# Performance work log

Measured on AMD Instinct MI355X. Metric: run time of the kernel, lower is better.

The kernel has to match this reference:

```python
import jax, jax.numpy as jnp
import numpy as np

DIM = 1024

def setup_inputs() -> dict:
    key = jax.random.key(0)
    k1, k2, k3, k4 = jax.random.split(key, 4)
    B, L, D = 32, 2048, DIM
    x = jax.random.normal(k1, (B, D), dtype=jnp.float32)
    context = jax.random.normal(k2, (B, L, D), dtype=jnp.float32)
    # linear_concatWa: Linear(2*dim, dim, bias=False) -> weight [dim, 2*dim]
    Wa = jax.random.normal(k3, (D, 2 * D), dtype=jnp.float32) * (1.0 / np.sqrt(2 * D))
    # linear_concatVa: Linear(dim, 1, bias=False) -> weight [1, dim]
    Va = jax.random.normal(k4, (1, D), dtype=jnp.float32) * (1.0 / np.sqrt(D))
    return {"x": x, "context": context, "Wa": Wa, "Va": Va}


def reference(x, context, Wa, Va):
    # concat-mode additive (Bahdanau) attention.
    # Wa @ cat(ht, hs) == ht @ Wa[:, :D].T + hs @ Wa[:, D:].T  (avoids materializing concat)
    D = x.shape[-1]
    Wa_t, Wa_s = Wa[:, :D], Wa[:, D:]              # each [D, D]
    ht_proj = jnp.einsum('bd,kd->bk', x, Wa_t)     # [B, D]
    hs_proj = jnp.einsum('bld,kd->blk', context, Wa_s)  # [B, L, D]
    hidden = jnp.tanh(ht_proj[:, None, :] + hs_proj)    # [B, L, D]
    scores = jnp.einsum('blk,ok->bl', hidden, Va)       # [B, L]  (Va: [1, D])
    attn = jax.nn.softmax(scores, axis=-1)               # [B, L]
    weighted = jnp.einsum('bl,bld->bd', attn, context)   # [B, D]
    return weighted, attn
```

## Files before the change

### kernel.cpp

```cpp
#include <hip/hip_runtime.h>
#include <hip/hip_bf16.h>
#include <cstdint>
#include <cstddef>

#define DIM 1024
#define B_SZ 32
#define L_SZ 2048

#define BM 128
#define BN 128

#define CVT_BLOCKS 8192
#define HT_BLOCKS  512
#define WA_BLOCKS  512

typedef __attribute__((ext_vector_type(8))) short bf16x8;
typedef __attribute__((ext_vector_type(4))) float floatx4;

static __device__ __forceinline__ unsigned cvt2_bf16_rne(float a, float b) {
    unsigned ua = __builtin_bit_cast(unsigned, a);
    unsigned ub = __builtin_bit_cast(unsigned, b);
    ua = (ua + 0x7FFFu + ((ua >> 16) & 1u)) >> 16;
    ub = (ub + 0x7FFFu + ((ub >> 16) & 1u)) >> 16;
    return ua | (ub << 16);
}

static __device__ __forceinline__ float bf2f(unsigned u16) {
    return __builtin_bit_cast(float, u16 << 16);
}

static __device__ __forceinline__ float tanh_fast(float x) {
    float e = __expf(2.0f * x);
    return 1.0f - 2.0f * __builtin_amdgcn_rcpf(e + 1.0f);
}

static __device__ __forceinline__ void gld_lds16(const void* g, void* lds) {
    __builtin_amdgcn_global_load_lds(
        (const __attribute__((address_space(1))) unsigned int*)g,
        (__attribute__((address_space(3))) unsigned int*)lds,
        16, 0, 0);
}

__global__ __launch_bounds__(256) void pre_kernel(
    const float* __restrict__ x, const float* __restrict__ ctx,
    const float* __restrict__ Wa,
    unsigned short* __restrict__ ctxB, unsigned short* __restrict__ WaB,
    float* __restrict__ ht, float* __restrict__ scores,
    float* __restrict__ weighted)
{
    const int bid = blockIdx.x, t = threadIdx.x;

    if (bid < CVT_BLOCKS) {
        const float4* c4 = (const float4*)ctx;
        uint2* o2 = (uint2*)ctxB;
        #pragma unroll
        for (int it = 0; it < 4; ++it) {
            const long g = ((long)it * CVT_BLOCKS + bid) * 512;
            const float4 a = c4[g + t];
            const float4 b = c4[g + 256 + t];
            o2[g + t]       = make_uint2(cvt2_bf16_rne(a.x, a.y), cvt2_bf16_rne(a.z, a.w));
            o2[g + 256 + t] = make_uint2(cvt2_bf16_rne(b.x, b.y), cvt2_bf16_rne(b.z, b.w));
        }
    } else if (bid < CVT_BLOCKS + HT_BLOCKS) {
        const int lb = bid - CVT_BLOCKS;
        const int gi = lb * 256 + t;
        if (gi < B_SZ * L_SZ) scores[gi] = 0.f;
        const int b = lb >> 4, kb = lb & 15;
        __shared__ float xs[DIM];
        for (int i = t; i < DIM; i += 256) xs[i] = x[b * DIM + i];
        __syncthreads();
        const int wave = t >> 6, lane = t & 63;
        const float4* xs4 = (const float4*)xs;
        for (int kk = 0; kk < 16; ++kk) {
            const int k = kb * 64 + wave * 16 + kk;
            const float4* wr = (const float4*)(Wa + (size_t)k * (2 * DIM));
            float s = 0.f;
            #pragma unroll
            for (int d = 0; d < DIM / 4; d += 64) {
                const float4 w4 = wr[d + lane];
                const float4 x4 = xs4[d + lane];
                s += w4.x * x4.x + w4.y * x4.y + w4.z * x4.z + w4.w * x4.w;
            }
            #pragma unroll
            for (int off = 32; off > 0; off >>= 1) s += __shfl_xor(s, off);
            if (lane == 0) ht[b * DIM + k] = s;
        }
    } else {
        const int lb = bid - CVT_BLOCKS - HT_BLOCKS;
        const int i = lb * 256 + t;
        if (i < B_SZ * DIM) weighted[i] = 0.f;
        const int k = i >> 7, dc = i & 127;
        const float* s = Wa + (size_t)k * (2 * DIM) + DIM + dc * 8;
        const float4 a = ((const float4*)s)[0];
        const float4 b4 = ((const float4*)s)[1];
        uint4 o;
        o.x = cvt2_bf16_rne(a.x, a.y);
        o.y = cvt2_bf16_rne(a.z, a.w);
        o.z = cvt2_bf16_rne(b4.x, b4.y);
        o.w = cvt2_bf16_rne(b4.z, b4.w);
        ((uint4*)(WaB + (size_t)k * DIM + dc * 8))[0] = o;
    }
}

__global__ __launch_bounds__(256) void gemm_score_bf16(
    const unsigned short* __restrict__ A, const unsigned short* __restrict__ Bm,
    const float* __restrict__ Va, const float* __restrict__ ht,
    float* __restrict__ scores)
{
    __shared__ __align__(16) unsigned short As[BM * 64];
    __shared__ __align__(16) unsigned short Bs[BN * 64];
    const int t = threadIdx.x;

    const int bid = blockIdx.x;
    const int logical = (bid & 7) * 512 + (bid >> 3);
    const int n0 = (logical & 7) * BN;
    const int m0 = (logical >> 3) * BM;

    const int lane = t & 63, wave = t >> 6;
    const int l15 = lane & 15, quad = lane >> 4;
    const int wm = (wave >> 1) * 64, wn = (wave & 1) * 64;

    const int lr = lane >> 3;
    const int lc = (lane & 7) ^ lr;
    const size_t aRow = (size_t)(m0 + wave * 32 + lr);
    const size_t bRow = (size_t)(n0 + wave * 32 + lr);

    floatx4 acc[4][4];
    #pragma unroll
    for (int i = 0; i < 4; ++i)
        #pragma unroll
        for (int j = 0; j < 4; ++j) acc[i][j] = (floatx4)0.f;

    for (int k0 = 0; k0 < DIM; k0 += 64) {
        #pragma unroll
        for (int q = 0; q < 4; ++q) {
            gld_lds16(A + (aRow + q * 8) * DIM + k0 + lc * 8,
                      &As[(wave * 32 + q * 8) * 64]);
            gld_lds16(Bm + (bRow + q * 8) * DIM + k0 + lc * 8,
                      &Bs[(wave * 32 + q * 8) * 64]);
        }
        __syncthreads();

        bf16x8 af[2][4], bv[2][4];
        #pragma unroll
        for (int kb = 0; kb < 2; ++kb) {
            #pragma unroll
            for (int i = 0; i < 4; ++i) {
                const int r = wm + i * 16 + l15;
                const int c = (kb * 4 + quad) ^ (r & 7);
                af[kb][i] = *(const bf16x8*)&As[r * 64 + c * 8];
            }
            #pragma unroll
            for (int j = 0; j < 4; ++j) {
                const int r = wn + j * 16 + l15;
                const int c = (kb * 4 + quad) ^ (r & 7);
                bv[kb][j] = *(const bf16x8*)&Bs[r * 64 + c * 8];
            }
        }
        #pragma unroll
        for (int kb = 0; kb < 2; ++kb)
            #pragma unroll
            for (int i = 0; i < 4; ++i)
                #pragma unroll
                for (int j = 0; j < 4; ++j)
                    acc[i][j] = __builtin_amdgcn_mfma_f32_16x16x32_bf16(
                        af[kb][i], bv[kb][j], acc[i][j], 0, 0, 0);
        __syncthreads();
    }

    const int bb = m0 >> 11;
    float htv[4], vav[4];
    #pragma unroll
    for (int j = 0; j < 4; ++j) {
        const int ng = n0 + wn + j * 16 + l15;
        htv[j] = ht[bb * DIM + ng];
        vav[j] = Va[ng];
    }
    #pragma unroll
    for (int i = 0; i < 4; ++i) {
        #pragma unroll
        for (int r = 0; r < 4; ++r) {
            float s = 0.f;
            #pragma unroll
            for (int j = 0; j < 4; ++j)
                s += tanh_fast(acc[i][j][r] + htv[j]) * vav[j];
            s += __shfl_xor(s, 8);
            s += __shfl_xor(s, 4);
            s += __shfl_xor(s, 2);
            s += __shfl_xor(s, 1);
            if (l15 == 0)
                atomicAdd(&scores[m0 + wm + i * 16 + quad * 4 + r], s);
        }
    }
}

__global__ __launch_bounds__(256) void stats_kernel(
    const float* __restrict__ scores, float* __restrict__ attn)
{
    const int b = blockIdx.x, t = threadIdx.x;
    const float* sc = scores + b * L_SZ;
    __shared__ float red[256];

    float m = -1e30f;
    for (int l = t; l < L_SZ; l += 256) m = fmaxf(m, sc[l]);
    red[t] = m; __syncthreads();
    for (int s = 128; s > 0; s >>= 1) { if (t < s) red[t] = fmaxf(red[t], red[t + s]); __syncthreads(); }
    m = red[0]; __syncthreads();
    float sum = 0.f;
    for (int l = t; l < L_SZ; l += 256) sum += __expf(sc[l] - m);
    red[t] = sum; __syncthreads();
    for (int s = 128; s > 0; s >>= 1) { if (t < s) red[t] += red[t + s]; __syncthreads(); }
    const float inv = 1.0f / red[0];

    for (int l = t; l < L_SZ; l += 256)
        attn[b * L_SZ + l] = __expf(sc[l] - m) * inv;
}

__global__ __launch_bounds__(256) void post_kernel(
    const float* __restrict__ attn, const unsigned short* __restrict__ ctxB,
    float* __restrict__ weighted)
{
    const int b = blockIdx.x, slice = blockIdx.y, t = threadIdx.x;
    __shared__ float att[128];
    const int l0 = slice * 128;
    if (t < 128) att[t] = attn[b * L_SZ + l0 + t];
    __syncthreads();

    const unsigned short* cb = ctxB + ((size_t)b * L_SZ + l0) * DIM + t * 4;
    float a0 = 0.f, a1 = 0.f, a2 = 0.f, a3 = 0.f;
    #pragma unroll 4
    for (int l = 0; l < 128; ++l) {
        const float a = att[l];
        const uint2 v = *(const uint2*)(cb + (size_t)l * DIM);
        a0 += a * bf2f(v.x & 0xFFFFu);
        a1 += a * bf2f(v.x >> 16);
        a2 += a * bf2f(v.y & 0xFFFFu);
        a3 += a * bf2f(v.y >> 16);
    }
    float* o = weighted + b * DIM + t * 4;
    atomicAdd(o + 0, a0);
    atomicAdd(o + 1, a1);
    atomicAdd(o + 2, a2);
    atomicAdd(o + 3, a3);
}

#define LDS_STRIDE 40
__global__ __launch_bounds__(256) void ht_kernel_fb(const float* __restrict__ x,
                                                    const float* __restrict__ Wa,
                                                    float* __restrict__ ht,
                                                    float* __restrict__ scores,
                                                    float* __restrict__ weighted) {
    const int b = blockIdx.x, kb = blockIdx.y, t = threadIdx.x;
    const int gidx = (b * 16 + kb) * 256 + t;
    if (gidx < B_SZ * L_SZ) scores[gidx] = 0.f;
    if (gidx < B_SZ * DIM) weighted[gidx] = 0.f;
    __shared__ float xs[DIM];
    for (int i = t; i < DIM; i += 256) xs[i] = x[b * DIM + i];
    __syncthreads();
    const int wave = t >> 6, lane = t & 63;
    for (int kk = 0; kk < 16; ++kk) {
        const int k = kb * 64 + wave * 16 + kk;
        const float* wr = Wa + (size_t)k * (2 * DIM);
        float s = 0.f;
        #pragma unroll
        for (int d = 0; d < DIM; d += 64) s += xs[d + lane] * wr[d + lane];
        #pragma unroll
        for (int off = 32; off > 0; off >>= 1) s += __shfl_xor(s, off);
        if (lane == 0) ht[b * DIM + k] = s;
    }
}

__global__ __launch_bounds__(256, 2) void gemm_score_kernel(
    const float* __restrict__ ctx, const float* __restrict__ Wa,
    const float* __restrict__ Va, const float* __restrict__ ht,
    float* __restrict__ scores)
{
    __shared__ unsigned short As[BM * LDS_STRIDE];
    __shared__ unsigned short Bs[BN * LDS_STRIDE];
    const int t = threadIdx.x;
    const int n0 = blockIdx.x * BN;
    const int m0 = blockIdx.y * BM;
    const int lane = t & 63, wave = t >> 6;
    const int l15 = lane & 15, quad = lane >> 4;
    const int wm = (wave >> 1) * 64, wn = (wave & 1) * 64;
    const int srow = t >> 3;
    const int scol = (t & 7) * 4;
    const float* aBase = ctx + (size_t)(m0 + srow) * DIM + scol;
    const float* bBase = Wa + (size_t)(n0 + srow) * (2 * DIM) + DIM + scol;

    floatx4 acc[4][4];
    #pragma unroll
    for (int i = 0; i < 4; ++i)
        #pragma unroll
        for (int j = 0; j < 4; ++j) acc[i][j] = (floatx4)0.f;

    for (int k0 = 0; k0 < DIM; k0 += 32) {
        __syncthreads();
        #pragma unroll
        for (int r = 0; r < 4; ++r) {
            const float4 va = *(const float4*)(aBase + (size_t)(r * 32) * DIM + k0);
            const float4 vb = *(const float4*)(bBase + (size_t)(r * 32) * (2 * DIM) + k0);
            *(uint2*)&As[(srow + r * 32) * LDS_STRIDE + scol] =
                make_uint2(cvt2_bf16_rne(va.x, va.y), cvt2_bf16_rne(va.z, va.w));
            *(uint2*)&Bs[(srow + r * 32) * LDS_STRIDE + scol] =
                make_uint2(cvt2_bf16_rne(vb.x, vb.y), cvt2_bf16_rne(vb.z, vb.w));
        }
        __syncthreads();
        bf16x8 af[4], bfr[4];
        #pragma unroll
        for (int i = 0; i < 4; ++i)
            af[i] = *(const bf16x8*)&As[(wm + i * 16 + l15) * LDS_STRIDE + quad * 8];
        #pragma unroll
        for (int j = 0; j < 4; ++j)
            bfr[j] = *(const bf16x8*)&Bs[(wn + j * 16 + l15) * LDS_STRIDE + quad * 8];
        #pragma unroll
        for (int i = 0; i < 4; ++i)
            #pragma unroll
            for (int j = 0; j < 4; ++j)
                acc[i][j] = __builtin_amdgcn_mfma_f32_16x16x32_bf16(af[i], bfr[j], acc[i][j], 0, 0, 0);
    }
    const int bb = m0 >> 11;
    float htv[4], vav[4];
    #pragma unroll
    for (int j = 0; j < 4; ++j) {
        const int ng = n0 + wn + j * 16 + l15;
        htv[j] = ht[bb * DIM + ng];
        vav[j] = Va[ng];
    }
    #pragma unroll
    for (int i = 0; i < 4; ++i) {
        #pragma unroll
        for (int r = 0; r < 4; ++r) {
            float s = 0.f;
            #pragma unroll
            for (int j = 0; j < 4; ++j)
                s += tanh_fast(acc[i][j][r] + htv[j]) * vav[j];
            s += __shfl_xor(s, 8);
            s += __shfl_xor(s, 4);
            s += __shfl_xor(s, 2);
            s += __shfl_xor(s, 1);
            if (l15 == 0)
                atomicAdd(&scores[m0 + wm + i * 16 + quad * 4 + r], s);
        }
    }
}

__global__ __launch_bounds__(256) void post_kernel_fb(
    const float* __restrict__ scores, const float* __restrict__ ctx,
    float* __restrict__ attn, float* __restrict__ weighted)
{
    const int b = blockIdx.x, slice = blockIdx.y, t = threadIdx.x;
    const float* sc = scores + b * L_SZ;
    __shared__ float red[256];
    __shared__ float att[128];
    float m = -1e30f;
    for (int l = t; l < L_SZ; l += 256) m = fmaxf(m, sc[l]);
    red[t] = m; __syncthreads();
    for (int s = 128; s > 0; s >>= 1) { if (t < s) red[t] = fmaxf(red[t], red[t + s]); __syncthreads(); }
    m = red[0]; __syncthreads();
    float sum = 0.f;
    for (int l = t; l < L_SZ; l += 256) sum += __expf(sc[l] - m);
    red[t] = sum; __syncthreads();
    for (int s = 128; s > 0; s >>= 1) { if (t < s) red[t] += red[t + s]; __syncthreads(); }
    const float inv = 1.0f / red[0];
    const int l0 = slice * 128;
    if (t < 128) {
        const float av = __expf(sc[l0 + t] - m) * inv;
        att[t] = av;
        attn[b * L_SZ + l0 + t] = av;
    }
    __syncthreads();
    const float* cb = ctx + ((size_t)b * L_SZ + l0) * DIM + t * 4;
    float4 w = make_float4(0.f, 0.f, 0.f, 0.f);
    for (int l = 0; l < 128; ++l) {
        const float a = att[l];
        const float4 c = *(const float4*)(cb + (size_t)l * DIM);
        w.x += a * c.x; w.y += a * c.y; w.z += a * c.z; w.w += a * c.w;
    }
    float* o = weighted + b * DIM + t * 4;
    atomicAdd(o + 0, w.x);
    atomicAdd(o + 1, w.y);
    atomicAdd(o + 2, w.z);
    atomicAdd(o + 3, w.w);
}

extern "C" void kernel_launch(void* const* d_in, const int* in_sizes, int n_in,
                              void* d_out, int out_size, void* d_ws, size_t ws_size,
                              hipStream_t stream) {
    const float* x   = (const float*)d_in[0];
    const float* ctx = (const float*)d_in[1];
    const float* Wa  = (const float*)d_in[2];
    const float* Va  = (const float*)d_in[3];

    float* out      = (float*)d_out;
    float* weighted = out;
    float* attn     = out + B_SZ * DIM;

    float* scores = (float*)d_ws;
    float* ht     = scores + B_SZ * L_SZ;

    const size_t base = (size_t)(B_SZ * L_SZ + B_SZ * DIM) * sizeof(float);
    const size_t need = base + (size_t)DIM * DIM * 2
                      + (size_t)B_SZ * L_SZ * DIM * 2;

    if (ws_size >= need) {
        unsigned short* WaB  = (unsigned short*)((char*)d_ws + base);
        unsigned short* ctxB = WaB + (size_t)DIM * DIM;
        pre_kernel<<<CVT_BLOCKS + HT_BLOCKS + WA_BLOCKS, 256, 0, stream>>>(
            x, ctx, Wa, ctxB, WaB, ht, scores, weighted);
        gemm_score_bf16<<<(DIM / BN) * ((B_SZ * L_SZ) / BM), 256, 0, stream>>>(
            ctxB, WaB, Va, ht, scores);
        stats_kernel<<<B_SZ, 256, 0, stream>>>(scores, attn);
        post_kernel<<<dim3(B_SZ, 16), 256, 0, stream>>>(attn, ctxB, weighted);
    } else {
        ht_kernel_fb<<<dim3(B_SZ, 16), 256, 0, stream>>>(x, Wa, ht, scores, weighted);
        gemm_score_kernel<<<dim3(DIM / BN, (B_SZ * L_SZ) / BM), 256, 0, stream>>>(
            ctx, Wa, Va, ht, scores);
        post_kernel_fb<<<dim3(B_SZ, 16), 256, 0, stream>>>(scores, ctx, attn, weighted);
    }
}
```

Baseline: 607.5 us.

## Double-buffer LDS tiles in bf16 score GEMM and drop block swizzle

Splits the GEMM's shared-memory tiles into two buffers, so global-to-LDS loads for the next K slice are issued before the MFMA work on the current slice. This hides load latency behind compute. It also removes the XCD-aware block index remapping and launches a plain 2D grid, which changes L2 locality across chiplets. The kernel now uses twice the LDS (64KB), which may lower occupancy.

```diff
diff --git a/kernel.cpp b/kernel.cpp
--- a/kernel.cpp
+++ b/kernel.cpp
@@ -102,20 +102,58 @@
     }
 }
 
+#define STAGE(AS, BS, K0)                                                     \
+    {                                                                         \
+        _Pragma("unroll")                                                     \
+        for (int q = 0; q < 4; ++q) {                                         \
+            gld_lds16(A + (aRow + q * 8) * DIM + (K0) + lc * 8,               \
+                      &AS[(wave * 32 + q * 8) * 64]);                         \
+            gld_lds16(Bm + (bRow + q * 8) * DIM + (K0) + lc * 8,              \
+                      &BS[(wave * 32 + q * 8) * 64]);                         \
+        }                                                                     \
+    }
+
+#define COMPUTE(AS, BS)                                                       \
+    {                                                                         \
+        bf16x8 af[2][4], bv[2][4];                                            \
+        _Pragma("unroll")                                                     \
+        for (int kb = 0; kb < 2; ++kb) {                                      \
+            _Pragma("unroll")                                                 \
+            for (int i = 0; i < 4; ++i) {                                     \
+                const int r = wm + i * 16 + l15;                              \
+                const int c = (kb * 4 + quad) ^ (r & 7);                      \
+                af[kb][i] = *(const bf16x8*)&AS[r * 64 + c * 8];              \
+            }                                                                 \
+            _Pragma("unroll")                                                 \
+            for (int j = 0; j < 4; ++j) {                                     \
+                const int r = wn + j * 16 + l15;                              \
+                const int c = (kb * 4 + quad) ^ (r & 7);                      \
+                bv[kb][j] = *(const bf16x8*)&BS[r * 64 + c * 8];              \
+            }                                                                 \
+        }                                                                     \
+        _Pragma("unroll")                                                     \
+        for (int kb = 0; kb < 2; ++kb)                                        \
+            _Pragma("unroll")                                                 \
+            for (int i = 0; i < 4; ++i)                                       \
+                _Pragma("unroll")                                             \
+                for (int j = 0; j < 4; ++j)                                   \
+                    acc[i][j] = __builtin_amdgcn_mfma_f32_16x16x32_bf16(      \
+                        af[kb][i], bv[kb][j], acc[i][j], 0, 0, 0);            \
+    }
+
 __global__ __launch_bounds__(256) void gemm_score_bf16(
     const unsigned short* __restrict__ A, const unsigned short* __restrict__ Bm,
     const float* __restrict__ Va, const float* __restrict__ ht,
     float* __restrict__ scores)
 {
-    __shared__ __align__(16) unsigned short As[BM * 64];
-    __shared__ __align__(16) unsigned short Bs[BN * 64];
+    __shared__ __align__(16) unsigned short As0[BM * 64];
+    __shared__ __align__(16) unsigned short Bs0[BN * 64];
+    __shared__ __align__(16) unsigned short As1[BM * 64];
+    __shared__ __align__(16) unsigned short Bs1[BN * 64];
+
     const int t = threadIdx.x;
-
-    const int bid = blockIdx.x;
-    const int logical = (bid & 7) * 512 + (bid >> 3);
-    const int n0 = (logical & 7) * BN;
-    const int m0 = (logical >> 3) * BM;
-
+    const int n0 = blockIdx.x * BN;
+    const int m0 = blockIdx.y * BM;
     const int lane = t & 63, wave = t >> 6;
     const int l15 = lane & 15, quad = lane >> 4;
     const int wm = (wave >> 1) * 64, wn = (wave & 1) * 64;
@@ -131,40 +169,16 @@
         #pragma unroll
         for (int j = 0; j < 4; ++j) acc[i][j] = (floatx4)0.f;
 
-    for (int k0 = 0; k0 < DIM; k0 += 64) {
-        #pragma unroll
-        for (int q = 0; q < 4; ++q) {
-            gld_lds16(A + (aRow + q * 8) * DIM + k0 + lc * 8,
-                      &As[(wave * 32 + q * 8) * 64]);
-            gld_lds16(Bm + (bRow + q * 8) * DIM + k0 + lc * 8,
-                      &Bs[(wave * 32 + q * 8) * 64]);
-        }
+    STAGE(As0, Bs0, 0);
+    __syncthreads();
+
+    #pragma unroll 1
+    for (int k0 = 0; k0 < DIM; k0 += 128) {
+        STAGE(As1, Bs1, k0 + 64);
+        COMPUTE(As0, Bs0);
         __syncthreads();
-
-        bf16x8 af[2][4], bv[2][4];
-        #pragma unroll
-        for (int kb = 0; kb < 2; ++kb) {
-            #pragma unroll
-            for (int i = 0; i < 4; ++i) {
-                const int r = wm + i * 16 + l15;
-                const int c = (kb * 4 + quad) ^ (r & 7);
-                af[kb][i] = *(const bf16x8*)&As[r * 64 + c * 8];
-            }
-            #pragma unroll
-            for (int j = 0; j < 4; ++j) {
-                const int r = wn + j * 16 + l15;
-                const int c = (kb * 4 + quad) ^ (r & 7);
-                bv[kb][j] = *(const bf16x8*)&Bs[r * 64 + c * 8];
-            }
-        }
-        #pragma unroll
-        for (int kb = 0; kb < 2; ++kb)
-            #pragma unroll
-            for (int i = 0; i < 4; ++i)
-                #pragma unroll
-                for (int j = 0; j < 4; ++j)
-                    acc[i][j] = __builtin_amdgcn_mfma_f32_16x16x32_bf16(
-                        af[kb][i], bv[kb][j], acc[i][j], 0, 0, 0);
+        if (k0 + 128 < DIM) STAGE(As0, Bs0, k0 + 128);
+        COMPUTE(As1, Bs1);
         __syncthreads();
     }
 
@@ -408,7 +422,7 @@
         unsigned short* ctxB = WaB + (size_t)DIM * DIM;
         pre_kernel<<<CVT_BLOCKS + HT_BLOCKS + WA_BLOCKS, 256, 0, stream>>>(
             x, ctx, Wa, ctxB, WaB, ht, scores, weighted);
-        gemm_score_bf16<<<(DIM / BN) * ((B_SZ * L_SZ) / BM), 256, 0, stream>>>(
+        gemm_score_bf16<<<dim3(DIM / BN, (B_SZ * L_SZ) / BM), 256, 0, stream>>>(
             ctxB, WaB, Va, ht, scores);
         stats_kernel<<<B_SZ, 256, 0, stream>>>(scores, attn);
         post_kernel<<<dim3(B_SZ, 16), 256, 0, stream>>>(attn, ctxB, weighted);
```

Measured after the change: 617.8 us. About the same (+1.7%).

## Widen post-kernel loads to 16 bytes, double its grid, drop GEMM block swizzle

Applied to the files above, without the earlier changes.

The weighted-sum kernel now has each thread load eight bf16 values per row with 16-byte loads. The two halves of the block split the rows of a 64-row slice, and their partial sums are combined in shared memory before the atomics. The grid doubles to 32 slices per batch to keep parallelism up. Separately, the GEMM drops its bid-to-tile swizzle in favour of a plain 2D grid, which changes tile launch order and may hurt L2 reuse of the weight and context tiles.

```diff
diff --git a/kernel.cpp b/kernel.cpp
--- a/kernel.cpp
+++ b/kernel.cpp
@@ -110,12 +110,8 @@
     __shared__ __align__(16) unsigned short As[BM * 64];
     __shared__ __align__(16) unsigned short Bs[BN * 64];
     const int t = threadIdx.x;
-
-    const int bid = blockIdx.x;
-    const int logical = (bid & 7) * 512 + (bid >> 3);
-    const int n0 = (logical & 7) * BN;
-    const int m0 = (logical >> 3) * BM;
-
+    const int n0 = blockIdx.x * BN;
+    const int m0 = blockIdx.y * BM;
     const int lane = t & 63, wave = t >> 6;
     const int l15 = lane & 15, quad = lane >> 4;
     const int wm = (wave >> 1) * 64, wn = (wave & 1) * 64;
@@ -221,27 +217,49 @@
     float* __restrict__ weighted)
 {
     const int b = blockIdx.x, slice = blockIdx.y, t = threadIdx.x;
-    __shared__ float att[128];
-    const int l0 = slice * 128;
-    if (t < 128) att[t] = attn[b * L_SZ + l0 + t];
+    __shared__ float att[64];
+    __shared__ float red2[128 * 8];
+    const int l0 = slice * 64;
+    if (t < 64) att[t] = attn[b * L_SZ + l0 + t];
     __syncthreads();
 
-    const unsigned short* cb = ctxB + ((size_t)b * L_SZ + l0) * DIM + t * 4;
+    const int dg = (t & 127) * 8;
+    const int lh = t >> 7;
+    const unsigned short* cb = ctxB + ((size_t)b * L_SZ + l0 + lh) * DIM + dg;
+
     float a0 = 0.f, a1 = 0.f, a2 = 0.f, a3 = 0.f;
-    #pragma unroll 4
-    for (int l = 0; l < 128; ++l) {
-        const float a = att[l];
-        const uint2 v = *(const uint2*)(cb + (size_t)l * DIM);
+    float a4 = 0.f, a5 = 0.f, a6 = 0.f, a7 = 0.f;
+    #pragma unroll 8
+    for (int j = 0; j < 32; ++j) {
+        const float a = att[lh + 2 * j];
+        const uint4 v = *(const uint4*)(cb + (size_t)(2 * j) * DIM);
         a0 += a * bf2f(v.x & 0xFFFFu);
         a1 += a * bf2f(v.x >> 16);
         a2 += a * bf2f(v.y & 0xFFFFu);
         a3 += a * bf2f(v.y >> 16);
-    }
-    float* o = weighted + b * DIM + t * 4;
-    atomicAdd(o + 0, a0);
-    atomicAdd(o + 1, a1);
-    atomicAdd(o + 2, a2);
-    atomicAdd(o + 3, a3);
+        a4 += a * bf2f(v.z & 0xFFFFu);
+        a5 += a * bf2f(v.z >> 16);
+        a6 += a * bf2f(v.w & 0xFFFFu);
+        a7 += a * bf2f(v.w >> 16);
+    }
+    if (lh == 1) {
+        float* r = &red2[(t & 127) * 8];
+        r[0] = a0; r[1] = a1; r[2] = a2; r[3] = a3;
+        r[4] = a4; r[5] = a5; r[6] = a6; r[7] = a7;
+    }
+    __syncthreads();
+    if (lh == 0) {
+        const float* r = &red2[t * 8];
+        float* o = weighted + b * DIM + dg;
+        atomicAdd(o + 0, a0 + r[0]);
+        atomicAdd(o + 1, a1 + r[1]);
+        atomicAdd(o + 2, a2 + r[2]);
+        atomicAdd(o + 3, a3 + r[3]);
+        atomicAdd(o + 4, a4 + r[4]);
+        atomicAdd(o + 5, a5 + r[5]);
+        atomicAdd(o + 6, a6 + r[6]);
+        atomicAdd(o + 7, a7 + r[7]);
+    }
 }
 
 #define LDS_STRIDE 40
@@ -408,10 +426,10 @@
         unsigned short* ctxB = WaB + (size_t)DIM * DIM;
         pre_kernel<<<CVT_BLOCKS + HT_BLOCKS + WA_BLOCKS, 256, 0, stream>>>(
             x, ctx, Wa, ctxB, WaB, ht, scores, weighted);
-        gemm_score_bf16<<<(DIM / BN) * ((B_SZ * L_SZ) / BM), 256, 0, stream>>>(
+        gemm_score_bf16<<<dim3(DIM / BN, (B_SZ * L_SZ) / BM), 256, 0, stream>>>(
             ctxB, WaB, Va, ht, scores);
         stats_kernel<<<B_SZ, 256, 0, stream>>>(scores, attn);
-        post_kernel<<<dim3(B_SZ, 16), 256, 0, stream>>>(attn, ctxB, weighted);
+        post_kernel<<<dim3(B_SZ, 32), 256, 0, stream>>>(attn, ctxB, weighted);
     } else {
         ht_kernel_fb<<<dim3(B_SZ, 16), 256, 0, stream>>>(x, Wa, ht, scores, weighted);
         gemm_score_kernel<<<dim3(DIM / BN, (B_SZ * L_SZ) / BM), 256, 0, stream>>>(
```

After: 622.6 us. 1.02x slower.
